# Optimization experiments

Hardware: AMD Instinct MI355X
Metric: run time of the kernel (lower is better)

The kernel has to match this reference:

```python
import math
import jax, jax.numpy as jnp
import numpy as np

B, H, L = 8, 512, 4096
N = 64 // 2  # d_state//2 complex pairs
DT_MIN, DT_MAX = 1e-3, 0.1


def setup_inputs() -> dict:
    key = jax.random.key(0)
    k_u, k_dt, k_C, k_D, k_W = jax.random.split(key, 5)
    u = jax.random.normal(k_u, (B, H, L), dtype=jnp.float32)
    log_dt = jax.random.uniform(k_dt, (H,), dtype=jnp.float32) * (
        math.log(DT_MAX) - math.log(DT_MIN)) + math.log(DT_MIN)
    log_A_real = jnp.log(0.5 * jnp.ones((H, N), dtype=jnp.float32))
    A_imag = math.pi * jnp.broadcast_to(jnp.arange(N, dtype=jnp.float32), (H, N))
    C = jax.random.normal(k_C, (H, N, 2), dtype=jnp.float32)  # view_as_real of cfloat
    D = jax.random.normal(k_D, (H,), dtype=jnp.float32)
    W_out = jax.random.normal(k_W, (2 * H, H), dtype=jnp.float32) * 0.05  # 1x1 conv weight
    b_out = jnp.zeros((2 * H,), dtype=jnp.float32)
    return {"u": u, "log_dt": log_dt, "log_A_real": log_A_real, "A_imag": A_imag,
            "C": C, "D": D, "W_out": W_out, "b_out": b_out}


def _ssm_kernel(log_dt, log_A_real, A_imag, C, length):
    dt = jnp.exp(log_dt)                             # (H,)
    A = -jnp.exp(log_A_real) + 1j * A_imag           # (H,N) complex
    dtA = A * dt[:, None]                            # (H,N)
    l = jnp.arange(length, dtype=jnp.float32)
    K = jnp.exp(dtA[:, :, None] * l)                 # (H,N,L) complex Vandermonde
    Cc = C[..., 0] + 1j * C[..., 1]                  # (H,N)
    Cs = Cc * (jnp.exp(dtA) - 1.0) / A               # (H,N)
    return 2.0 * jnp.einsum('hn,hnl->hl', Cs, K).real  # (H,L) real kernel


def reference(u, log_dt, log_A_real, A_imag, C, D, W_out, b_out):
    length = u.shape[-1]
    k = _ssm_kernel(log_dt, log_A_real, A_imag, C, length)  # (H,L)
    n_fft = 2 * length
    k_f = jnp.fft.rfft(k, n=n_fft)                   # (H, L+1)
    u_f = jnp.fft.rfft(u, n=n_fft)                   # (B,H,L+1)
    y = jnp.fft.irfft(u_f * k_f, n=n_fft)[..., :length]  # FFT convolution
    y = y + u * D[:, None]                           # D skip connection
    y = jax.nn.gelu(y, approximate=False)            # torch nn.GELU = exact erf
    y = jnp.einsum('oh,bhl->bol', W_out, y) + b_out[:, None]  # 1x1 conv
    a, b = jnp.split(y, 2, axis=-2)                  # GLU over channel dim
    return a * jax.nn.sigmoid(b)
```

## Files before the change

kernel.cpp:

```cpp
#include <hip/hip_runtime.h>
#include <math.h>

constexpr int cB = 8, cH = 512, cL = 4096, cN = 32;
constexpr int cG = 32, cLC = 128;
constexpr int cHN = cH * cN;

constexpr size_t OF_RR  = 0;
constexpr size_t OF_RI  = (size_t)cHN;
constexpr size_t OF_RPR = (size_t)2*cHN;
constexpr size_t OF_RPI = (size_t)3*cHN;
constexpr size_t OF_C2R = (size_t)4*cHN;
constexpr size_t OF_C2I = (size_t)5*cHN;
constexpr size_t OF_DR  = (size_t)6*cHN;
constexpr size_t OF_DI  = (size_t)7*cHN;
constexpr size_t OF_K   = (size_t)8*cHN;
constexpr size_t OF_WP  = OF_K + (size_t)512*128;
constexpr size_t OF_A   = OF_WP + (size_t)1024*512/2;
constexpr size_t OF_V   = OF_A + (size_t)512*128*192/2;
constexpr size_t OF_XP  = OF_V + (size_t)512*64*128/2;
constexpr size_t OF_G   = OF_XP + (size_t)512*256*64/2;
constexpr size_t OF_GT  = OF_A;

typedef __bf16 bf16x8 __attribute__((ext_vector_type(8)));
typedef float  f32x4  __attribute__((ext_vector_type(4)));

static __device__ __forceinline__ ushort f2bf(float x) {
    unsigned u = __float_as_uint(x);
    unsigned r = (u + 0x7fffu + ((u >> 16) & 1u)) >> 16;
    return (ushort)r;
}
static __device__ __forceinline__ float bf2f(ushort v) {
    return __uint_as_float(((unsigned)v) << 16);
}
static __device__ __forceinline__ unsigned pk2(float a, float b) {
    return (unsigned)f2bf(a) | ((unsigned)f2bf(b) << 16);
}
static __device__ __forceinline__ float gelu(float v) {
    return 0.5f * v * (1.0f + erff(v * 0.70710678118654752f));
}
static __device__ __forceinline__ void gload16(const void* g, void* l) {
    __builtin_amdgcn_global_load_lds(
        (const __attribute__((address_space(1))) unsigned*)g,
        (__attribute__((address_space(3))) unsigned*)l, 16, 0, 0);
}

__global__ void k_consts(const float* __restrict__ log_dt,
                         const float* __restrict__ log_A_real,
                         const float* __restrict__ A_imag,
                         const float* __restrict__ Cin,
                         float* __restrict__ ws)
{
    int tid = blockIdx.x * 256 + threadIdx.x;
    if (tid >= cHN) return;
    int h = tid >> 5;
    float dt = expf(log_dt[h]);
    float Ar = -expf(log_A_real[tid]);
    float Ai = A_imag[tid];
    float dr = dt * Ar, di = dt * Ai;
    float er = expf(dr);
    float rr = er * cosf(di), ri = er * sinf(di);
    float erL = expf(dr * (float)cLC);
    float diL = di * (float)cLC;
    float rpr = erL * cosf(diL), rpi = erL * sinf(diL);
    float cr = Cin[2*tid], ci = Cin[2*tid+1];
    float nr = rr - 1.0f, ni = ri;
    float inv = 1.0f / (Ar*Ar + Ai*Ai);
    float wr = (nr*Ar + ni*Ai) * inv;
    float wi = (ni*Ar - nr*Ai) * inv;
    float csr = cr*wr - ci*wi;
    float csi = cr*wi + ci*wr;
    ws[OF_RR  + tid] = rr;  ws[OF_RI  + tid] = ri;
    ws[OF_RPR + tid] = rpr; ws[OF_RPI + tid] = rpi;
    ws[OF_C2R + tid] = 2.0f*csr; ws[OF_C2I + tid] = 2.0f*csi;
    ws[OF_DR  + tid] = dr;  ws[OF_DI  + tid] = di;
}

__global__ void k_pack_w(const float* __restrict__ W, ushort* __restrict__ Wp)
{
    int idx = blockIdx.x * 256 + threadIdx.x;
    int base = idx * 4;
    int m = base >> 9;
    int k = base & 511;
    int src = (m & 1) ? (512 + (m >> 1)) : (m >> 1);
    float4 v = *(const float4*)&W[(size_t)src * 512 + k];
    ushort4 o;
    o.x = f2bf(v.x); o.y = f2bf(v.y); o.z = f2bf(v.z); o.w = f2bf(v.w);
    *(ushort4*)&Wp[base] = o;
}

__global__ void k_vmat(const float* __restrict__ ws, ushort* __restrict__ wsu)
{
    int tid = blockIdx.x * 256 + threadIdx.x;
    int h = tid >> 5, n = tid & 31;
    float dr = ws[OF_DR + tid], di = ws[OF_DI + tid];
    float e127 = expf(dr * 127.f), a127 = di * 127.f;
    float pr = e127 * cosf(a127), pi_ = e127 * sinf(a127);
    float rie = expf(-dr);
    float rc = rie * cosf(di), rs = -rie * sinf(di);
    ushort* vre = wsu + 2*OF_V + ((size_t)h*64 + n) * 128;
    ushort* vim = wsu + 2*OF_V + ((size_t)h*64 + 32 + n) * 128;
    for (int j4 = 0; j4 < 128; j4 += 4) {
        ushort4 r4, i4;
        #pragma unroll
        for (int e = 0; e < 4; ++e) {
            ((ushort*)&r4)[e] = f2bf(pr);
            ((ushort*)&i4)[e] = f2bf(pi_);
            float npr = pr*rc - pi_*rs;
            float npi = pr*rs + pi_*rc;
            pr = npr; pi_ = npi;
        }
        *(ushort4*)&vre[j4] = r4;
        *(ushort4*)&vim[j4] = i4;
    }
}

__global__ void k_emat(const float* __restrict__ ws, float* __restrict__ wsf,
                       ushort* __restrict__ wsu)
{
    int tid = blockIdx.x * 256 + threadIdx.x;
    int h = tid >> 7, l = tid & 127;
    float fl = (float)l, fl1 = (float)(l + 1);
    const float* dr_ = ws + OF_DR + (size_t)h*32;
    const float* di_ = ws + OF_DI + (size_t)h*32;
    const float* c2r_ = ws + OF_C2R + (size_t)h*32;
    const float* c2i_ = ws + OF_C2I + (size_t)h*32;
    ushort* rowA = wsu + 2*OF_A + ((size_t)h*128 + l) * 192;
    float kacc = 0.f;
    for (int n4 = 0; n4 < 32; n4 += 4) {
        ushort4 prq, npq;
        #pragma unroll
        for (int e = 0; e < 4; ++e) {
            int n = n4 + e;
            float dr = dr_[n], di = di_[n], c2r = c2r_[n], c2i = c2i_[n];
            float e0 = expf(dr * fl), a0 = di * fl;
            float c0 = cosf(a0), s0 = sinf(a0);
            kacc += e0 * (c2r*c0 - c2i*s0);
            float e1 = expf(dr * fl1), a1 = di * fl1;
            float c1 = cosf(a1), s1 = sinf(a1);
            ((ushort*)&prq)[e] = f2bf(e1 * (c2r*c1 - c2i*s1));
            ((ushort*)&npq)[e] = f2bf(-e1 * (c2r*s1 + c2i*c1));
        }
        *(ushort4*)&rowA[128 + n4] = prq;
        *(ushort4*)&rowA[160 + n4] = npq;
    }
    wsf[OF_K + (size_t)h*128 + l] = kacc;
}

__global__ void k_build_T(const float* __restrict__ wsf, const float* __restrict__ Dvec,
                          ushort* __restrict__ wsu)
{
    __shared__ float kv[256];
    int t = threadIdx.x;
    int tid = blockIdx.x * 256 + t;
    int h = tid >> 7, l = tid & 127;
    kv[t] = wsf[OF_K + (size_t)blockIdx.x * 256 + t];
    __syncthreads();
    const float* krow = kv + ((t >> 7) << 7);
    float Dh = Dvec[h];
    ushort* row = wsu + 2*OF_A + ((size_t)h*128 + l) * 192;
    for (int j8 = 0; j8 < 128; j8 += 8) {
        uint4 q;
        unsigned w[4];
        #pragma unroll
        for (int p = 0; p < 4; ++p) {
            int j0 = j8 + 2*p, j1 = j0 + 1;
            float v0 = (j0 <= l) ? krow[l - j0] : 0.f;
            float v1 = (j1 <= l) ? krow[l - j1] : 0.f;
            if (j0 == l) v0 += Dh;
            if (j1 == l) v1 += Dh;
            w[p] = pk2(v0, v1);
        }
        q.x = w[0]; q.y = w[1]; q.z = w[2]; q.w = w[3];
        *(uint4*)&row[j8] = q;
    }
}

__global__ __launch_bounds__(256) void k_state_gemm(const float* __restrict__ u,
                                                    const ushort* __restrict__ wsu,
                                                    ushort* __restrict__ xp)
{
    __shared__ ushort Vs[64 * 136];
    __shared__ ushort Bs[256 * 40];
    const int t = threadIdx.x;
    const int h = blockIdx.x;
    const int wn = t >> 6, lane = t & 63;
    const int lm = lane & 15, q = lane >> 4;

    {
        int idx = t * 32;
        int row = idx >> 7, kk = idx & 127;
        const ushort* src = wsu + 2*OF_V + ((size_t)h*64 + row) * 128 + kk;
        uint4 v0 = *(const uint4*)&src[0],  v1 = *(const uint4*)&src[8];
        uint4 v2 = *(const uint4*)&src[16], v3 = *(const uint4*)&src[24];
        ushort* d = (ushort*)Vs + row * 136 + kk;
        *(uint4*)&d[0] = v0; *(uint4*)&d[8] = v1;
        *(uint4*)&d[16] = v2; *(uint4*)&d[24] = v3;
    }

    const int b = t >> 5, c = t & 31;
    f32x4 acc[4][4];
    #pragma unroll
    for (int i = 0; i < 4; ++i)
        #pragma unroll
        for (int j = 0; j < 4; ++j) acc[i][j] = (f32x4){0.f,0.f,0.f,0.f};

    for (int k0 = 0; k0 < 128; k0 += 32) {
        const float* up = u + ((size_t)(b*cH + h)) * cL + (size_t)c*128 + k0;
        float4 f[8];
        #pragma unroll
        for (int e = 0; e < 8; ++e) f[e] = *(const float4*)&up[4*e];
        __syncthreads();
        ushort* d = (ushort*)Bs + t * 40;
        #pragma unroll
        for (int e = 0; e < 4; ++e) {
            uint4 w;
            w.x = pk2(f[2*e].x, f[2*e].y);   w.y = pk2(f[2*e].z, f[2*e].w);
            w.z = pk2(f[2*e+1].x, f[2*e+1].y); w.w = pk2(f[2*e+1].z, f[2*e+1].w);
            *(uint4*)&d[8*e] = w;
        }
        __syncthreads();
        bf16x8 af[4], bfr[4];
        #pragma unroll
        for (int mi = 0; mi < 4; ++mi)
            af[mi] = *(const bf16x8*)&Vs[(16*mi + lm) * 136 + k0 + 8*q];
        #pragma unroll
        for (int ni = 0; ni < 4; ++ni)
            bfr[ni] = *(const bf16x8*)&Bs[(64*wn + 16*ni + lm) * 40 + 8*q];
        #pragma unroll
        for (int mi = 0; mi < 4; ++mi)
            #pragma unroll
            for (int ni = 0; ni < 4; ++ni)
                acc[mi][ni] = __builtin_amdgcn_mfma_f32_16x16x32_bf16(af[mi], bfr[ni], acc[mi][ni], 0,0,0);
    }
    #pragma unroll
    for (int mi = 0; mi < 4; ++mi)
        #pragma unroll
        for (int ni = 0; ni < 4; ++ni) {
            int col = 64*wn + 16*ni + lm;
            int comp = 16*mi + 4*q;
            ushort4 st;
            st.x = f2bf(acc[mi][ni][0]); st.y = f2bf(acc[mi][ni][1]);
            st.z = f2bf(acc[mi][ni][2]); st.w = f2bf(acc[mi][ni][3]);
            *(ushort4*)&xp[((size_t)h*256 + col) * 64 + comp] = st;
        }
}

__global__ __launch_bounds__(256) void k_scan2(const float* __restrict__ ws,
                                               ushort* __restrict__ xp)
{
    int tid = blockIdx.x * 256 + threadIdx.x;
    int n  = tid & 31;
    int bh = tid >> 5;
    int h  = bh & (cH - 1);
    int b  = bh >> 9;
    float rpr = ws[OF_RPR + (size_t)h*32 + n];
    float rpi = ws[OF_RPI + (size_t)h*32 + n];
    float Xr = 0.f, Xi = 0.f;
    ushort* base = xp + ((size_t)h*256 + (size_t)b*32) * 64 + n;
    for (int c = 0; c < cG; ++c) {
        ushort* p = base + (size_t)c * 64;
        float sr = bf2f(p[0]), si = bf2f(p[32]);
        p[0]  = f2bf(Xr);
        p[32] = f2bf(Xi);
        float nXr = fmaf(rpr, Xr, fmaf(-rpi, Xi, sr));
        float nXi = fmaf(rpr, Xi, fmaf(rpi, Xr, si));
        Xr = nXr; Xi = nXi;
    }
}

__global__ __launch_bounds__(256) void k_conv(const float* __restrict__ u,
                                              const ushort* __restrict__ wsu,
                                              ushort* __restrict__ g)
{
    __shared__ ushort As[128 * 40];
    __shared__ ushort Bs[128 * 40];
    const int t = threadIdx.x;
    const int ctile = blockIdx.x;
    const int h = blockIdx.y;
    const int wave = t >> 6, lane = t & 63;
    const int wm = wave & 1, wn = wave >> 1;
    const int lm = lane & 15, q = lane >> 4;

    const int arow = t & 127, ah = t >> 7;
    const int col = arow, half = ah;
    const int gc = ctile * 128 + col;
    const int ub = gc >> 5, uc = gc & 31;

    const ushort* Ab = wsu + 2*OF_A + ((size_t)h*128 + arow) * 192;
    const ushort* xpB = wsu + 2*OF_XP + ((size_t)h*256 + gc) * 64;

    f32x4 acc[4][4];
    #pragma unroll
    for (int i = 0; i < 4; ++i)
        #pragma unroll
        for (int j = 0; j < 4; ++j) acc[i][j] = (f32x4){0.f,0.f,0.f,0.f};

    for (int k0 = 0; k0 < 192; k0 += 32) {
        uint4 a0 = *(const uint4*)&Ab[k0 + 16*ah];
        uint4 a1 = *(const uint4*)&Ab[k0 + 16*ah + 8];
        uint4 b0, b1;
        if (k0 < 128) {
            const float* up = u + ((size_t)(ub*cH + h)) * cL + (size_t)uc*128 + k0 + 16*half;
            float4 f0 = *(const float4*)&up[0],  f1 = *(const float4*)&up[4];
            float4 f2 = *(const float4*)&up[8],  f3 = *(const float4*)&up[12];
            b0.x = pk2(f0.x,f0.y); b0.y = pk2(f0.z,f0.w);
            b0.z = pk2(f1.x,f1.y); b0.w = pk2(f1.z,f1.w);
            b1.x = pk2(f2.x,f2.y); b1.y = pk2(f2.z,f2.w);
            b1.z = pk2(f3.x,f3.y); b1.w = pk2(f3.z,f3.w);
        } else {
            const ushort* xs = xpB + (k0 - 128) + 16*half;
            b0 = *(const uint4*)&xs[0];
            b1 = *(const uint4*)&xs[8];
        }
        __syncthreads();
        *(uint4*)&As[arow*40 + 16*ah]     = a0;
        *(uint4*)&As[arow*40 + 16*ah + 8] = a1;
        *(uint4*)&Bs[col*40 + 16*half]     = b0;
        *(uint4*)&Bs[col*40 + 16*half + 8] = b1;
        __syncthreads();
        bool skip = (wm == 0) && (k0 == 64 || k0 == 96);
        if (!skip) {
            bf16x8 af[4], bfr[4];
            #pragma unroll
            for (int mi = 0; mi < 4; ++mi)
                af[mi] = *(const bf16x8*)&As[(64*wm + 16*mi + lm) * 40 + 8*q];
            #pragma unroll
            for (int ni = 0; ni < 4; ++ni)
                bfr[ni] = *(const bf16x8*)&Bs[(64*wn + 16*ni + lm) * 40 + 8*q];
            #pragma unroll
            for (int mi = 0; mi < 4; ++mi)
                #pragma unroll
                for (int ni = 0; ni < 4; ++ni)
                    acc[mi][ni] = __builtin_amdgcn_mfma_f32_16x16x32_bf16(af[mi], bfr[ni], acc[mi][ni], 0,0,0);
        }
    }
    #pragma unroll
    for (int ni = 0; ni < 4; ++ni) {
        int ocol = ctile*128 + 64*wn + 16*ni + lm;
        int ob = ocol >> 5, oc = ocol & 31;
        ushort* grow = g + ((size_t)(ob*cH + h)) * cL + (size_t)oc*128;
        #pragma unroll
        for (int mi = 0; mi < 4; ++mi) {
            int l = 64*wm + 16*mi + 4*q;
            ushort4 st;
            st.x = f2bf(gelu(acc[mi][ni][0]));
            st.y = f2bf(gelu(acc[mi][ni][1]));
            st.z = f2bf(gelu(acc[mi][ni][2]));
            st.w = f2bf(gelu(acc[mi][ni][3]));
            *(ushort4*)&grow[l] = st;
        }
    }
}

__global__ __launch_bounds__(256) void k_transpose(const ushort* __restrict__ gsrc,
                                                   ushort* __restrict__ gT)
{
    __shared__ ushort tile[64 * 64];
    const int t = threadIdx.x;
    const int b  = blockIdx.z;
    const int h0 = blockIdx.y << 6;
    const int l0 = blockIdx.x << 6;
    const ushort* gb = gsrc + ((size_t)b * cH + h0) * cL + l0;
    const int lb = t & 7;
    #pragma unroll
    for (int half = 0; half < 2; ++half) {
        int r = (t >> 3) + half * 32;
        uint4 v = *(const uint4*)&gb[(size_t)r * cL + lb * 8];
        int sb = lb ^ (r & 7) ^ (r >> 3);
        *(uint4*)&tile[r * 64 + sb * 8] = v;
    }
    __syncthreads();
    ushort* gTb = gT + ((size_t)b * cL + l0) * cH + h0;
    #pragma unroll
    for (int half = 0; half < 2; ++half) {
        int l  = (t >> 3) + half * 32;
        int hb = t & 7;
        ushort vals[8];
        #pragma unroll
        for (int e = 0; e < 8; ++e) {
            int r  = hb * 8 + e;
            int sb = (l >> 3) ^ (r & 7) ^ (r >> 3);
            vals[e] = tile[r * 64 + sb * 8 + (l & 7)];
        }
        *(uint4*)&gTb[(size_t)l * cH + hb * 8] = *(uint4*)vals;
    }
}

__global__ __launch_bounds__(256) void k_gemm2(const ushort* __restrict__ Wp,
                                               const float* __restrict__ bias,
                                               const ushort* __restrict__ gT,
                                               float* __restrict__ out)
{
    __shared__ ushort As[2][128 * 32];
    __shared__ ushort Bs[2][128 * 32];
    const int t    = threadIdx.x;
    const int l0   = blockIdx.x * 128;
    const int by   = blockIdx.y;
    const int b    = blockIdx.z;
    const int wave = t >> 6, lane = t & 63;
    const int wm   = wave & 1, wn = wave >> 1;
    const int lm   = lane & 15, q = lane >> 4;

    const int srow = lane >> 2;
    const int scol = (lane & 3) * 8;
    const ushort* Ag = Wp + (size_t)(by * 128) * 512;
    const ushort* Bg = gT + ((size_t)b * cL + l0) * 512;

    f32x4 acc[4][4];
    #pragma unroll
    for (int i = 0; i < 4; ++i)
        #pragma unroll
        for (int j = 0; j < 4; ++j)
            acc[i][j] = (f32x4){0.f, 0.f, 0.f, 0.f};

    auto stage = [&](ushort* Asb, ushort* Bsb, int k0) {
        #pragma unroll
        for (int j = 0; j < 2; ++j) {
            int row = 32*wave + 16*j + srow;
            gload16(Ag + (size_t)row * 512 + k0 + scol,
                    (char*)Asb + wave*2048 + j*1024);
            gload16(Bg + (size_t)row * 512 + k0 + scol,
                    (char*)Bsb + wave*2048 + j*1024);
        }
    };
    auto compute = [&](const ushort* Asb, const ushort* Bsb) {
        bf16x8 af[4], bfr[4];
        #pragma unroll
        for (int mi = 0; mi < 4; ++mi)
            af[mi] = *(const bf16x8*)&Asb[(64*wm + 16*mi + lm) * 32 + 8*q];
        #pragma unroll
        for (int ni = 0; ni < 4; ++ni)
            bfr[ni] = *(const bf16x8*)&Bsb[(64*wn + 16*ni + lm) * 32 + 8*q];
        #pragma unroll
        for (int mi = 0; mi < 4; ++mi)
            #pragma unroll
            for (int ni = 0; ni < 4; ++ni)
                acc[mi][ni] = __builtin_amdgcn_mfma_f32_16x16x32_bf16(af[mi], bfr[ni], acc[mi][ni], 0,0,0);
    };

    stage(As[0], Bs[0], 0);
    __syncthreads();
    int cur = 0;
    for (int ks = 0; ks < 15; ++ks) {
        stage(As[cur ^ 1], Bs[cur ^ 1], (ks + 1) * 32);
        compute(As[cur], Bs[cur]);
        __syncthreads();
        cur ^= 1;
    }
    compute(As[cur], Bs[cur]);

    const int obase = by * 64 + 32 * wm;
    #pragma unroll
    for (int mi = 0; mi < 4; ++mi) {
        #pragma unroll
        for (int p = 0; p < 2; ++p) {
            int o = obase + 8*mi + 2*q + p;
            float ba = bias[o], bb = bias[512 + o];
            float* orow = out + ((size_t)b * cH + o) * cL + l0 + 64*wn + lm;
            #pragma unroll
            for (int ni = 0; ni < 4; ++ni) {
                float av = acc[mi][ni][2*p]     + ba;
                float gv = acc[mi][ni][2*p + 1] + bb;
                orow[16 * ni] = av / (1.f + expf(-gv));
            }
        }
    }
}

extern "C" void kernel_launch(void* const* d_in, const int* in_sizes, int n_in,
                              void* d_out, int out_size, void* d_ws, size_t ws_size,
                              hipStream_t stream)
{
    (void)in_sizes; (void)n_in; (void)out_size; (void)ws_size;
    const float* u          = (const float*)d_in[0];
    const float* log_dt     = (const float*)d_in[1];
    const float* log_A_real = (const float*)d_in[2];
    const float* A_imag     = (const float*)d_in[3];
    const float* C          = (const float*)d_in[4];
    const float* D          = (const float*)d_in[5];
    const float* W          = (const float*)d_in[6];
    const float* bias       = (const float*)d_in[7];
    float* out = (float*)d_out;
    float* ws  = (float*)d_ws;
    ushort* wsu = (ushort*)d_ws;
    ushort* Wp  = wsu + 2*OF_WP;
    ushort* xp  = wsu + 2*OF_XP;
    ushort* gbf = wsu + 2*OF_G;
    ushort* gTu = wsu + 2*OF_GT;

    hipLaunchKernelGGL(k_consts, dim3(cHN/256), dim3(256), 0, stream,
                       log_dt, log_A_real, A_imag, C, ws);
    hipLaunchKernelGGL(k_pack_w, dim3(1024*512/4/256), dim3(256), 0, stream, W, Wp);
    hipLaunchKernelGGL(k_vmat, dim3(cHN/256), dim3(256), 0, stream, ws, wsu);
    hipLaunchKernelGGL(k_emat, dim3(512*128/256), dim3(256), 0, stream, ws, ws, wsu);
    hipLaunchKernelGGL(k_build_T, dim3(512*128/256), dim3(256), 0, stream, ws, D, wsu);
    hipLaunchKernelGGL(k_state_gemm, dim3(512), dim3(256), 0, stream, u, wsu, xp);
    hipLaunchKernelGGL(k_scan2, dim3(cB*cH*cN/256), dim3(256), 0, stream, ws, xp);
    hipLaunchKernelGGL(k_conv, dim3(2, 512), dim3(256), 0, stream, u, wsu, gbf);
    hipLaunchKernelGGL(k_transpose, dim3(cL/64, cH/64, cB), dim3(256), 0, stream, gbf, gTu);
    hipLaunchKernelGGL(k_gemm2, dim3(cL/128, 1024/128, cB), dim3(256), 0, stream,
                       Wp, bias, gTu, out);
}
```

Before: 290.9 us.

## Fuse setup kernels and triple-buffer swizzled LDS pipeline in output GEMM

```diff
diff --git a/kernel.cpp b/kernel.cpp
--- a/kernel.cpp
+++ b/kernel.cpp
@@ -44,15 +44,16 @@
         (__attribute__((address_space(3))) unsigned*)l, 16, 0, 0);
 }
 
-__global__ void k_consts(const float* __restrict__ log_dt,
-                         const float* __restrict__ log_A_real,
-                         const float* __restrict__ A_imag,
-                         const float* __restrict__ Cin,
-                         float* __restrict__ ws)
+__global__ void k_consts_vmat(const float* __restrict__ log_dt,
+                              const float* __restrict__ log_A_real,
+                              const float* __restrict__ A_imag,
+                              const float* __restrict__ Cin,
+                              float* __restrict__ ws,
+                              ushort* __restrict__ wsu)
 {
     int tid = blockIdx.x * 256 + threadIdx.x;
     if (tid >= cHN) return;
-    int h = tid >> 5;
+    int h = tid >> 5, n = tid & 31;
     float dt = expf(log_dt[h]);
     float Ar = -expf(log_A_real[tid]);
     float Ai = A_imag[tid];
@@ -73,6 +74,26 @@
     ws[OF_RPR + tid] = rpr; ws[OF_RPI + tid] = rpi;
     ws[OF_C2R + tid] = 2.0f*csr; ws[OF_C2I + tid] = 2.0f*csi;
     ws[OF_DR  + tid] = dr;  ws[OF_DI  + tid] = di;
+
+    float e127 = expf(dr * 127.f), a127 = di * 127.f;
+    float pr = e127 * cosf(a127), pi_ = e127 * sinf(a127);
+    float rie = expf(-dr);
+    float rc = rie * cosf(di), rs = -rie * sinf(di);
+    ushort* vre = wsu + 2*OF_V + ((size_t)h*64 + n) * 128;
+    ushort* vim = wsu + 2*OF_V + ((size_t)h*64 + 32 + n) * 128;
+    for (int j4 = 0; j4 < 128; j4 += 4) {
+        ushort4 r4, i4;
+        #pragma unroll
+        for (int e = 0; e < 4; ++e) {
+            ((ushort*)&r4)[e] = f2bf(pr);
+            ((ushort*)&i4)[e] = f2bf(pi_);
+            float npr = pr*rc - pi_*rs;
+            float npi = pr*rs + pi_*rc;
+            pr = npr; pi_ = npi;
+        }
+        *(ushort4*)&vre[j4] = r4;
+        *(ushort4*)&vim[j4] = i4;
+    }
 }
 
 __global__ void k_pack_w(const float* __restrict__ W, ushort* __restrict__ Wp)
@@ -88,36 +109,12 @@
     *(ushort4*)&Wp[base] = o;
 }
 
-__global__ void k_vmat(const float* __restrict__ ws, ushort* __restrict__ wsu)
-{
-    int tid = blockIdx.x * 256 + threadIdx.x;
-    int h = tid >> 5, n = tid & 31;
-    float dr = ws[OF_DR + tid], di = ws[OF_DI + tid];
-    float e127 = expf(dr * 127.f), a127 = di * 127.f;
-    float pr = e127 * cosf(a127), pi_ = e127 * sinf(a127);
-    float rie = expf(-dr);
-    float rc = rie * cosf(di), rs = -rie * sinf(di);
-    ushort* vre = wsu + 2*OF_V + ((size_t)h*64 + n) * 128;
-    ushort* vim = wsu + 2*OF_V + ((size_t)h*64 + 32 + n) * 128;
-    for (int j4 = 0; j4 < 128; j4 += 4) {
-        ushort4 r4, i4;
-        #pragma unroll
-        for (int e = 0; e < 4; ++e) {
-            ((ushort*)&r4)[e] = f2bf(pr);
-            ((ushort*)&i4)[e] = f2bf(pi_);
-            float npr = pr*rc - pi_*rs;
-            float npi = pr*rs + pi_*rc;
-            pr = npr; pi_ = npi;
-        }
-        *(ushort4*)&vre[j4] = r4;
-        *(ushort4*)&vim[j4] = i4;
-    }
-}
-
-__global__ void k_emat(const float* __restrict__ ws, float* __restrict__ wsf,
+__global__ void k_embt(const float* __restrict__ ws, const float* __restrict__ Dvec,
                        ushort* __restrict__ wsu)
 {
-    int tid = blockIdx.x * 256 + threadIdx.x;
+    __shared__ float kv[256];
+    int t = threadIdx.x;
+    int tid = blockIdx.x * 256 + t;
     int h = tid >> 7, l = tid & 127;
     float fl = (float)l, fl1 = (float)(l + 1);
     const float* dr_ = ws + OF_DR + (size_t)h*32;
@@ -143,21 +140,10 @@
         *(ushort4*)&rowA[128 + n4] = prq;
         *(ushort4*)&rowA[160 + n4] = npq;
     }
-    wsf[OF_K + (size_t)h*128 + l] = kacc;
-}
-
-__global__ void k_build_T(const float* __restrict__ wsf, const float* __restrict__ Dvec,
-                          ushort* __restrict__ wsu)
-{
-    __shared__ float kv[256];
-    int t = threadIdx.x;
-    int tid = blockIdx.x * 256 + t;
-    int h = tid >> 7, l = tid & 127;
-    kv[t] = wsf[OF_K + (size_t)blockIdx.x * 256 + t];
+    kv[t] = kacc;
     __syncthreads();
     const float* krow = kv + ((t >> 7) << 7);
     float Dh = Dvec[h];
-    ushort* row = wsu + 2*OF_A + ((size_t)h*128 + l) * 192;
     for (int j8 = 0; j8 < 128; j8 += 8) {
         uint4 q;
         unsigned w[4];
@@ -171,7 +157,7 @@
             w[p] = pk2(v0, v1);
         }
         q.x = w[0]; q.y = w[1]; q.z = w[2]; q.w = w[3];
-        *(uint4*)&row[j8] = q;
+        *(uint4*)&rowA[j8] = q;
     }
 }
 
@@ -391,8 +377,8 @@
                                                const ushort* __restrict__ gT,
                                                float* __restrict__ out)
 {
-    __shared__ ushort As[2][128 * 32];
-    __shared__ ushort Bs[2][128 * 32];
+    __shared__ ushort As[3][128 * 32];
+    __shared__ ushort Bs[3][128 * 32];
     const int t    = threadIdx.x;
     const int l0   = blockIdx.x * 128;
     const int by   = blockIdx.y;
@@ -401,8 +387,9 @@
     const int wm   = wave & 1, wn = wave >> 1;
     const int lm   = lane & 15, q = lane >> 4;
 
-    const int srow = lane >> 2;
-    const int scol = (lane & 3) * 8;
+    const int srow  = lane >> 2;
+    const int sw_st = (((lane & 3) ^ ((srow >> 1) & 3)) * 8);
+    const int sw_rd = ((q ^ ((lm >> 1) & 3)) * 8);
     const ushort* Ag = Wp + (size_t)(by * 128) * 512;
     const ushort* Bg = gT + ((size_t)b * cL + l0) * 512;
 
@@ -413,24 +400,25 @@
         for (int j = 0; j < 4; ++j)
             acc[i][j] = (f32x4){0.f, 0.f, 0.f, 0.f};
 
-    auto stage = [&](ushort* Asb, ushort* Bsb, int k0) {
+    auto stage = [&](int bi, int kt) {
+        const int k0 = kt * 32;
         #pragma unroll
         for (int j = 0; j < 2; ++j) {
             int row = 32*wave + 16*j + srow;
-            gload16(Ag + (size_t)row * 512 + k0 + scol,
-                    (char*)Asb + wave*2048 + j*1024);
-            gload16(Bg + (size_t)row * 512 + k0 + scol,
-                    (char*)Bsb + wave*2048 + j*1024);
+            gload16(Ag + (size_t)row * 512 + k0 + sw_st,
+                    (char*)&As[bi][0] + wave*2048 + j*1024);
+            gload16(Bg + (size_t)row * 512 + k0 + sw_st,
+                    (char*)&Bs[bi][0] + wave*2048 + j*1024);
         }
     };
-    auto compute = [&](const ushort* Asb, const ushort* Bsb) {
+    auto compute = [&](int bi) {
         bf16x8 af[4], bfr[4];
         #pragma unroll
         for (int mi = 0; mi < 4; ++mi)
-            af[mi] = *(const bf16x8*)&Asb[(64*wm + 16*mi + lm) * 32 + 8*q];
+            af[mi] = *(const bf16x8*)&As[bi][(64*wm + 16*mi + lm) * 32 + sw_rd];
         #pragma unroll
         for (int ni = 0; ni < 4; ++ni)
-            bfr[ni] = *(const bf16x8*)&Bsb[(64*wn + 16*ni + lm) * 32 + 8*q];
+            bfr[ni] = *(const bf16x8*)&Bs[bi][(64*wn + 16*ni + lm) * 32 + sw_rd];
         #pragma unroll
         for (int mi = 0; mi < 4; ++mi)
             #pragma unroll
@@ -438,16 +426,31 @@
                 acc[mi][ni] = __builtin_amdgcn_mfma_f32_16x16x32_bf16(af[mi], bfr[ni], acc[mi][ni], 0,0,0);
     };
 
-    stage(As[0], Bs[0], 0);
-    __syncthreads();
-    int cur = 0;
-    for (int ks = 0; ks < 15; ++ks) {
-        stage(As[cur ^ 1], Bs[cur ^ 1], (ks + 1) * 32);
-        compute(As[cur], Bs[cur]);
-        __syncthreads();
-        cur ^= 1;
-    }
-    compute(As[cur], Bs[cur]);
+    stage(0, 0);
+    stage(1, 1);
+    int c0 = 0, c1 = 1, c2 = 2;
+    for (int ks = 0; ks < 14; ++ks) {
+        stage(c2, ks + 2);
+        asm volatile("s_waitcnt vmcnt(8)" ::: "memory");
+        __builtin_amdgcn_s_barrier();
+        asm volatile("" ::: "memory");
+        __builtin_amdgcn_sched_barrier(0);
+        compute(c0);
+        asm volatile("" ::: "memory");
+        __builtin_amdgcn_sched_barrier(0);
+        __builtin_amdgcn_s_barrier();
+        int tmp = c0; c0 = c1; c1 = c2; c2 = tmp;
+    }
+    asm volatile("s_waitcnt vmcnt(4)" ::: "memory");
+    __builtin_amdgcn_s_barrier();
+    asm volatile("" ::: "memory");
+    __builtin_amdgcn_sched_barrier(0);
+    compute(c0);
+    asm volatile("s_waitcnt vmcnt(0)" ::: "memory");
+    __builtin_amdgcn_s_barrier();
+    asm volatile("" ::: "memory");
+    __builtin_amdgcn_sched_barrier(0);
+    compute(c1);
 
     const int obase = by * 64 + 32 * wm;
     #pragma unroll
@@ -488,12 +491,10 @@
     ushort* gbf = wsu + 2*OF_G;
     ushort* gTu = wsu + 2*OF_GT;
 
-    hipLaunchKernelGGL(k_consts, dim3(cHN/256), dim3(256), 0, stream,
-                       log_dt, log_A_real, A_imag, C, ws);
+    hipLaunchKernelGGL(k_consts_vmat, dim3(cHN/256), dim3(256), 0, stream,
+                       log_dt, log_A_real, A_imag, C, ws, wsu);
     hipLaunchKernelGGL(k_pack_w, dim3(1024*512/4/256), dim3(256), 0, stream, W, Wp);
-    hipLaunchKernelGGL(k_vmat, dim3(cHN/256), dim3(256), 0, stream, ws, wsu);
-    hipLaunchKernelGGL(k_emat, dim3(512*128/256), dim3(256), 0, stream, ws, ws, wsu);
-    hipLaunchKernelGGL(k_build_T, dim3(512*128/256), dim3(256), 0, stream, ws, D, wsu);
+    hipLaunchKernelGGL(k_embt, dim3(512*128/256), dim3(256), 0, stream, ws, D, wsu);
     hipLaunchKernelGGL(k_state_gemm, dim3(512), dim3(256), 0, stream, u, wsu, xp);
     hipLaunchKernelGGL(k_scan2, dim3(cB*cH*cN/256), dim3(256), 0, stream, ws, xp);
     hipLaunchKernelGGL(k_conv, dim3(2, 512), dim3(256), 0, stream, u, wsu, gbf);
```

Measured after the change: 288.9 us. Within noise of the previous version (-0.7%).
